# Kernel optimization log

Hardware: AMD Instinct MI355X
Metric: run time of the kernel (lower is better)

Reference implementation:

```python
import jax, jax.numpy as jnp
import numpy as np

H = 2048   # hidden_dim
E = 8      # num_experts
K = 2      # top_k
N = 4096   # tokens


def setup_inputs() -> dict:
    key = jax.random.key(0)
    ks = jax.random.split(key, 8)
    scale = 0.02
    return {
        "x": jax.random.normal(ks[0], (N, H), dtype=jnp.float32),
        # gate: torch Linear(H, E) -> weight [E, H], bias [E]
        "gate_W": jax.random.normal(ks[1], (E, H), dtype=jnp.float32) * scale,
        "gate_b": jnp.zeros((E,), dtype=jnp.float32),
        # per-expert 2-layer MLP; stored as [E, in, out] for direct einsum
        "W1": jax.random.normal(ks[2], (E, H, H), dtype=jnp.float32) * scale,
        "b1": jnp.zeros((E, H), dtype=jnp.float32),
        "W2": jax.random.normal(ks[3], (E, H, H), dtype=jnp.float32) * scale,
        "b2": jnp.zeros((E, H), dtype=jnp.float32),
    }


def reference(x, gate_W, gate_b, W1, b1, W2, b2):
    # gate softmax over experts: [N, E]
    gate_scores = jax.nn.softmax(x @ gate_W.T + gate_b, axis=-1)
    topk_scores, topk_idx = jax.lax.top_k(gate_scores, K)  # [N, K]
    n = x.shape[0]
    # combine weights: score at selected experts, 0 elsewhere -> [N, E]
    combine = jnp.zeros_like(gate_scores).at[
        jnp.arange(n)[:, None], topk_idx
    ].set(topk_scores)
    # dense per-expert MLP: h [N, E, H]
    h = jax.nn.relu(jnp.einsum('nh,ehf->nef', x, W1) + b1)
    out_e = jnp.einsum('nef,efg->neg', h, W2) + b2  # [N, E, H]
    aggregated = jnp.einsum('ne,neh->nh', combine, out_e)  # [N, H]
    return aggregated, gate_scores
```

## Files before the change

### kernel.cpp

```cpp
#include <hip/hip_runtime.h>
#include <hip/hip_bf16.h>

#define N_TOK 4096
#define HD    2048
#define NE    8

#define BM 128
#define BN 256
#define BK 32
#define NKS (HD/BK)
#define MAXROWS (N_TOK*2 + NE*BM)
#define TMAX (MAXROWS/BM)
#define NNT  (HD/BN)
#define NWG  (TMAX*NNT)
#define TSZ  ((BM+BN)*BK*2)

#define NCOPY 64

typedef __attribute__((ext_vector_type(4))) float f32x4;
typedef __attribute__((ext_vector_type(8))) short short8;
typedef __attribute__((ext_vector_type(8))) unsigned short ushort8;

typedef unsigned short u16;
typedef unsigned int   u32;


__device__ __forceinline__ float bf2f(u16 u) {
  union { u32 i; float f; } c; c.i = ((u32)u) << 16; return c.f;
}
__device__ __forceinline__ u16 f2bf(float f) {
  u32 x = __float_as_uint(f);
  u32 r = (x + 0x7fffu + ((x >> 16) & 1u)) >> 16;
  return (u16)r;
}

__device__ __forceinline__ void gload_lds16(const void* gsrc, void* ldst) {
  __builtin_amdgcn_global_load_lds(
      (const __attribute__((address_space(1))) u32*)gsrc,
      (__attribute__((address_space(3))) u32*)ldst, 16, 0, 0);
}

__global__ __launch_bounds__(256) void convert_transpose_kernel(
    const float* __restrict__ W1, const float* __restrict__ W2,
    u16* __restrict__ W1T, u16* __restrict__ W2T) {
  __shared__ float tile[64][257];
  int z = blockIdx.z;
  const float* W = (z < NE) ? W1 : W2;
  u16* WT = (z < NE) ? W1T : W2T;
  int e = z & 7;
  size_t ebase = (size_t)e * HD * HD;
  int n0 = blockIdx.x * 256;
  int k0 = blockIdx.y * 64;
  int t = threadIdx.x;
  int l = t & 63, w = t >> 6;
  #pragma unroll
  for (int i = 0; i < 16; ++i) {
    int r = i*4 + w;
    f32x4 v = *reinterpret_cast<const f32x4*>(W + ebase + (size_t)(k0 + r) * HD + n0 + l*4);
    tile[r][l*4+0] = v[0]; tile[r][l*4+1] = v[1];
    tile[r][l*4+2] = v[2]; tile[r][l*4+3] = v[3];
  }
  __syncthreads();
  #pragma unroll
  for (int i = 0; i < 8; ++i) {
    int np = i*32 + (t >> 3);
    int kc = (t & 7) * 8;
    ushort8 v;
    #pragma unroll
    for (int j = 0; j < 8; ++j) v[j] = f2bf(tile[kc + j][np]);
    *reinterpret_cast<ushort8*>(WT + ebase + (size_t)(n0 + np) * HD + k0 + kc) = v;
  }
}

__global__ __launch_bounds__(256) void gate_kernel(
    const float* __restrict__ x, const float* __restrict__ gW, const float* __restrict__ gb,
    float* __restrict__ gate_out, int* __restrict__ cnt,
    int* __restrict__ picks, float* __restrict__ wts) {
  int wid = (blockIdx.x << 2) + (threadIdx.x >> 6);
  int lane = threadIdx.x & 63;
  int copy = blockIdx.x & (NCOPY-1);
  const float* xr = x + (size_t)wid * HD;
  float s[NE] = {};
  for (int k = 0; k < HD; k += 256) {
    f32x4 xv = *reinterpret_cast<const f32x4*>(xr + k + lane*4);
    #pragma unroll
    for (int e = 0; e < NE; ++e) {
      f32x4 wv = *reinterpret_cast<const f32x4*>(gW + (size_t)e*HD + k + lane*4);
      s[e] += xv[0]*wv[0] + xv[1]*wv[1] + xv[2]*wv[2] + xv[3]*wv[3];
    }
  }
  #pragma unroll
  for (int e = 0; e < NE; ++e) {
    float v = s[e];
    #pragma unroll
    for (int off = 32; off > 0; off >>= 1) v += __shfl_xor(v, off);
    s[e] = v + gb[e];
  }
  float mx = s[0];
  #pragma unroll
  for (int e = 1; e < NE; ++e) mx = fmaxf(mx, s[e]);
  float sum = 0.f;
  #pragma unroll
  for (int e = 0; e < NE; ++e) { s[e] = expf(s[e] - mx); sum += s[e]; }
  float inv = 1.f / sum;
  #pragma unroll
  for (int e = 0; e < NE; ++e) s[e] *= inv;
  int e0 = 0; float v0 = s[0];
  #pragma unroll
  for (int e = 1; e < NE; ++e) if (s[e] > v0) { v0 = s[e]; e0 = e; }
  int e1 = -1; float v1 = -1.f;
  #pragma unroll
  for (int e = 0; e < NE; ++e) if (e != e0 && s[e] > v1) { v1 = s[e]; e1 = e; }
  if (lane == 0) {
    #pragma unroll
    for (int e = 0; e < NE; ++e) gate_out[(size_t)wid*NE + e] = s[e];
    int p0 = atomicAdd(&cnt[copy*8 + e0], 1);
    int p1 = atomicAdd(&cnt[copy*8 + e1], 1);
    picks[wid*2]   = (p0 << 9) | (copy << 3) | e0;
    picks[wid*2+1] = (p1 << 9) | (copy << 3) | e1;
    wts[wid*2]   = v0;
    wts[wid*2+1] = v1;
  }
}

__global__ void scan_kernel(int* meta) {
  int e = threadIdx.x;
  if (e < NE) {
    int run = 0;
    for (int c = 0; c < NCOPY; ++c) {
      meta[512 + c*8 + e] = run;
      run += meta[c*8 + e];
    }
    meta[1024 + e] = run;
  }
}

__global__ void fill_kernel(const int* __restrict__ picks, const int* __restrict__ meta,
                            int* __restrict__ slot, int* __restrict__ rowTok) {
  int i = blockIdx.x * 256 + threadIdx.x;
  if (i >= N_TOK*2) return;
  int p = picks[i];
  int e = p & 7, c = (p >> 3) & (NCOPY-1), pos = p >> 9;
  int base = 0;
  #pragma unroll
  for (int ee = 0; ee < NE; ++ee)
    if (ee < e) base += ((meta[1024+ee] + BM - 1) >> 7) << 7;
  int row = base + meta[512 + c*8 + e] + pos;
  slot[i] = row;
  rowTok[row] = i >> 1;
}

__global__ __launch_bounds__(256) void gather_kernel(
    const float* __restrict__ x, const int* __restrict__ rowTok,
    u16* __restrict__ Xg) {
  int row = blockIdx.x;
  int tok = rowTok[row];
  int c = threadIdx.x * 8;
  ushort8 v;
  if (tok >= 0) {
    const f32x4* src = reinterpret_cast<const f32x4*>(x + (size_t)tok * HD + c);
    f32x4 a = src[0], b = src[1];
    #pragma unroll
    for (int j = 0; j < 4; ++j) { v[j] = f2bf(a[j]); v[4+j] = f2bf(b[j]); }
  } else {
    #pragma unroll
    for (int j = 0; j < 8; ++j) v[j] = 0;
  }
  *reinterpret_cast<ushort8*>(Xg + (size_t)row * HD + c) = v;
}

__device__ __forceinline__ void stage_tile(char* ldsbuf, const u16* Ak, const u16* Bk, int tid) {
  {
    int r = tid >> 2;
    int c = (tid & 3) ^ ((r >> 1) & 3);
    gload_lds16(Ak + (size_t)r*HD + c*8, ldsbuf + tid*16);
  }
  #pragma unroll
  for (int i = 0; i < 2; ++i) {
    int L = i*512 + tid;
    int r = L >> 2;
    int c = (L & 3) ^ ((r >> 1) & 3);
    gload_lds16(Bk + (size_t)r*HD + c*8, ldsbuf + BM*BK*2 + L*16);
  }
}

__device__ __forceinline__ void compute_ktile(
    const char* ldsA, const char* ldsB, f32x4 (&acc)[4][4],
    int wr, int wc, int l15, int lhi) {
  short8 af[4], bfr[4];
  #pragma unroll
  for (int m = 0; m < 4; ++m) {
    int r = wr*64 + m*16 + l15;
    int c = lhi ^ ((r >> 1) & 3);
    af[m] = *reinterpret_cast<const short8*>(ldsA + r*64 + c*16);
  }
  #pragma unroll
  for (int n = 0; n < 4; ++n) {
    int r = wc*64 + n*16 + l15;
    int c = lhi ^ ((r >> 1) & 3);
    bfr[n] = *reinterpret_cast<const short8*>(ldsB + r*64 + c*16);
  }
  #pragma unroll
  for (int m = 0; m < 4; ++m)
    #pragma unroll
    for (int n = 0; n < 4; ++n)
      acc[m][n] = __builtin_amdgcn_mfma_f32_16x16x32_bf16(af[m], bfr[n], acc[m][n], 0, 0, 0);
}

template<bool RELU>
__global__ __launch_bounds__(512, 4) void moe_gemm_kernel(
    const u16* __restrict__ A,
    const u16* __restrict__ WT,
    const float* __restrict__ bias,
    u16* __restrict__ Out,
    const int* __restrict__ tot) {
  int bid = blockIdx.x;
  int wg = (bid & 7) * (NWG/8) + (bid >> 3);
  int t  = wg >> 3;
  int nt = wg & 7;
  int tiles = 0, rows = 0, e = 0, tstart = 0, rbase = 0;
  #pragma unroll
  for (int i = 0; i < NE; ++i) {
    int tl = (tot[i] + BM - 1) >> 7;
    if (t >= tiles && t < tiles + tl) { e = i; tstart = tiles; rbase = rows; }
    tiles += tl; rows += tl << 7;
  }
  if (t >= tiles) return;
  int rowBase = rbase + (t - tstart) * BM;

  const u16* Ap = A + (size_t)rowBase * HD;
  const u16* Bp = WT + ((size_t)e * HD + (size_t)nt * BN) * HD;

  __shared__ char lds[3*TSZ];

  int tid = threadIdx.x;
  int lane = tid & 63;
  int wv = tid >> 6;
  int wr = wv >> 2, wc = wv & 3;
  int l15 = lane & 15, lhi = lane >> 4;

  f32x4 acc[4][4] = {};

  stage_tile(lds,       Ap,      Bp,      tid);
  stage_tile(lds + TSZ, Ap + BK, Bp + BK, tid);

  int rd = 0;
  for (int ks = 0; ks < NKS - 2; ++ks) {
    asm volatile("s_waitcnt vmcnt(3)" ::: "memory");
    __builtin_amdgcn_s_barrier();
    int wi = rd + 2; if (wi >= 3) wi -= 3;
    stage_tile(lds + wi*TSZ, Ap + (ks+2)*BK, Bp + (ks+2)*BK, tid);
    __builtin_amdgcn_sched_barrier(0);
    compute_ktile(lds + rd*TSZ, lds + rd*TSZ + BM*BK*2, acc, wr, wc, l15, lhi);
    if (++rd == 3) rd = 0;
  }
  asm volatile("s_waitcnt vmcnt(3)" ::: "memory");
  __builtin_amdgcn_s_barrier();
  compute_ktile(lds + rd*TSZ, lds + rd*TSZ + BM*BK*2, acc, wr, wc, l15, lhi);
  if (++rd == 3) rd = 0;
  asm volatile("s_waitcnt vmcnt(0)" ::: "memory");
  __builtin_amdgcn_s_barrier();
  compute_ktile(lds + rd*TSZ, lds + rd*TSZ + BM*BK*2, acc, wr, wc, l15, lhi);

  int orow = rowBase + wr*64;
  int ocol = nt*BN + wc*64;
  const float* bp = bias + (size_t)e * HD + ocol;
  #pragma unroll
  for (int n = 0; n < 4; ++n) {
    float bv = bp[n*16 + l15];
    #pragma unroll
    for (int m = 0; m < 4; ++m) {
      #pragma unroll
      for (int j = 0; j < 4; ++j) {
        float v = acc[m][n][j] + bv;
        if (RELU) v = fmaxf(v, 0.f);
        Out[(size_t)(orow + m*16 + lhi*4 + j) * HD + (ocol + n*16 + l15)] = f2bf(v);
      }
    }
  }
}

__global__ __launch_bounds__(256) void combine_kernel(
    const u16* __restrict__ Y, const int* __restrict__ slot,
    const float* __restrict__ wts, float* __restrict__ out) {
  int n = blockIdx.x;
  int r0 = slot[n*2], r1 = slot[n*2+1];
  float w0 = wts[n*2], w1 = wts[n*2+1];
  int c = threadIdx.x * 8;
  ushort8 y0 = *reinterpret_cast<const ushort8*>(Y + (size_t)r0*HD + c);
  ushort8 y1 = *reinterpret_cast<const ushort8*>(Y + (size_t)r1*HD + c);
  f32x4 o0, o1;
  #pragma unroll
  for (int j = 0; j < 4; ++j) {
    o0[j] = w0*bf2f(y0[j])   + w1*bf2f(y1[j]);
    o1[j] = w0*bf2f(y0[4+j]) + w1*bf2f(y1[4+j]);
  }
  f32x4* dst = reinterpret_cast<f32x4*>(out + (size_t)n*HD + c);
  dst[0] = o0; dst[1] = o1;
}

extern "C" void kernel_launch(void* const* d_in, const int* in_sizes, int n_in,
                              void* d_out, int out_size, void* d_ws, size_t ws_size,
                              hipStream_t stream) {
  const float* x     = (const float*)d_in[0];
  const float* gateW = (const float*)d_in[1];
  const float* gateb = (const float*)d_in[2];
  const float* W1    = (const float*)d_in[3];
  const float* b1    = (const float*)d_in[4];
  const float* W2    = (const float*)d_in[5];
  const float* b2    = (const float*)d_in[6];
  float* out      = (float*)d_out;
  float* gate_out = out + (size_t)N_TOK * HD;

  char* ws = (char*)d_ws;
  size_t o = 0;
  u16* W1T = (u16*)(ws + o); o += (size_t)NE*HD*HD*2;
  u16* W2T = (u16*)(ws + o); o += (size_t)NE*HD*HD*2;
  u16* Xg  = (u16*)(ws + o);
  u16* Y   = Xg;
  o += (size_t)MAXROWS*HD*2;
  u16* Hbuf = (u16*)(ws + o); o += (size_t)MAXROWS*HD*2;
  int*   meta   = (int*)(ws + o);   o += 8192;
  int*   picks  = (int*)(ws + o);   o += (size_t)N_TOK*2*4;
  float* wts    = (float*)(ws + o); o += (size_t)N_TOK*2*4;
  int*   slot   = (int*)(ws + o);   o += (size_t)N_TOK*2*4;
  int*   rowTok = (int*)(ws + o);   o += (size_t)MAXROWS*4;

  hipMemsetAsync(meta, 0, NCOPY*8*4, stream);
  hipMemsetAsync(rowTok, 0xFF, (size_t)MAXROWS*4, stream);

  convert_transpose_kernel<<<dim3(HD/256, HD/64, 2*NE), 256, 0, stream>>>(W1, W2, W1T, W2T);
  gate_kernel<<<N_TOK/4, 256, 0, stream>>>(x, gateW, gateb, gate_out, meta, picks, wts);
  scan_kernel<<<1, 64, 0, stream>>>(meta);
  fill_kernel<<<(N_TOK*2)/256, 256, 0, stream>>>(picks, meta, slot, rowTok);
  gather_kernel<<<MAXROWS, 256, 0, stream>>>(x, rowTok, Xg);
  moe_gemm_kernel<true ><<<dim3(NWG), 512, 0, stream>>>(Xg,   W1T, b1, Hbuf, meta + 1024);
  moe_gemm_kernel<false><<<dim3(NWG), 512, 0, stream>>>(Hbuf, W2T, b2, Y,    meta + 1024);
  combine_kernel<<<N_TOK, 256, 0, stream>>>(Y, slot, wts, out);
}
```

Baseline: 323.7 us.

## Fuse weighted combine into second expert GEMM via atomic scatter-add

The separate combine kernel is removed. The second expert GEMM now multiplies each output row by its routing weight and atomically adds the result into the fp32 output at the token's row, which requires zeroing the output buffer with a memset first. This avoids writing and re-reading the bf16 intermediate Y and drops one launch, at the cost of many scattered fp32 atomics and nondeterministic summation order. Separately, the gate kernel now stages the gate weights in LDS before use.

After: 375.8 us. 16.1% more time.

```diff
diff --git a/kernel.cpp b/kernel.cpp
--- a/kernel.cpp
+++ b/kernel.cpp
@@ -76,8 +76,17 @@
     const float* __restrict__ x, const float* __restrict__ gW, const float* __restrict__ gb,
     float* __restrict__ gate_out, int* __restrict__ cnt,
     int* __restrict__ picks, float* __restrict__ wts) {
-  int wid = (blockIdx.x << 2) + (threadIdx.x >> 6);
-  int lane = threadIdx.x & 63;
+  __shared__ float gwl[NE*HD];
+  int tid = threadIdx.x;
+  {
+    const f32x4* g4 = reinterpret_cast<const f32x4*>(gW);
+    f32x4* l4 = reinterpret_cast<f32x4*>(gwl);
+    #pragma unroll
+    for (int i = 0; i < 16; ++i) l4[i*256 + tid] = g4[i*256 + tid];
+  }
+  __syncthreads();
+  int wid = (blockIdx.x << 2) + (tid >> 6);
+  int lane = tid & 63;
   int copy = blockIdx.x & (NCOPY-1);
   const float* xr = x + (size_t)wid * HD;
   float s[NE] = {};
@@ -85,7 +94,7 @@
     f32x4 xv = *reinterpret_cast<const f32x4*>(xr + k + lane*4);
     #pragma unroll
     for (int e = 0; e < NE; ++e) {
-      f32x4 wv = *reinterpret_cast<const f32x4*>(gW + (size_t)e*HD + k + lane*4);
+      f32x4 wv = *reinterpret_cast<const f32x4*>(&gwl[e*HD + k + lane*4]);
       s[e] += xv[0]*wv[0] + xv[1]*wv[1] + xv[2]*wv[2] + xv[3]*wv[3];
     }
   }
@@ -136,7 +145,8 @@
 }
 
 __global__ void fill_kernel(const int* __restrict__ picks, const int* __restrict__ meta,
-                            int* __restrict__ slot, int* __restrict__ rowTok) {
+                            const float* __restrict__ wts,
+                            float* __restrict__ rowW, int* __restrict__ rowTok) {
   int i = blockIdx.x * 256 + threadIdx.x;
   if (i >= N_TOK*2) return;
   int p = picks[i];
@@ -146,7 +156,7 @@
   for (int ee = 0; ee < NE; ++ee)
     if (ee < e) base += ((meta[1024+ee] + BM - 1) >> 7) << 7;
   int row = base + meta[512 + c*8 + e] + pos;
-  slot[i] = row;
+  rowW[row] = wts[i];
   rowTok[row] = i >> 1;
 }
 
@@ -207,13 +217,16 @@
       acc[m][n] = __builtin_amdgcn_mfma_f32_16x16x32_bf16(af[m], bfr[n], acc[m][n], 0, 0, 0);
 }
 
-template<bool RELU>
+template<int MODE>
 __global__ __launch_bounds__(512, 4) void moe_gemm_kernel(
     const u16* __restrict__ A,
     const u16* __restrict__ WT,
     const float* __restrict__ bias,
     u16* __restrict__ Out,
-    const int* __restrict__ tot) {
+    const int* __restrict__ tot,
+    const int* __restrict__ rowTok,
+    const float* __restrict__ rowW,
+    float* __restrict__ fout) {
   int bid = blockIdx.x;
   int wg = (bid & 7) * (NWG/8) + (bid >> 3);
   int t  = wg >> 3;
@@ -265,38 +278,45 @@
   int orow = rowBase + wr*64;
   int ocol = nt*BN + wc*64;
   const float* bp = bias + (size_t)e * HD + ocol;
-  #pragma unroll
-  for (int n = 0; n < 4; ++n) {
-    float bv = bp[n*16 + l15];
-    #pragma unroll
-    for (int m = 0; m < 4; ++m) {
+
+  if (MODE == 0) {
+    #pragma unroll
+    for (int n = 0; n < 4; ++n) {
+      float bv = bp[n*16 + l15];
+      #pragma unroll
+      for (int m = 0; m < 4; ++m) {
+        #pragma unroll
+        for (int j = 0; j < 4; ++j) {
+          float v = fmaxf(acc[m][n][j] + bv, 0.f);
+          Out[(size_t)(orow + m*16 + lhi*4 + j) * HD + (ocol + n*16 + l15)] = f2bf(v);
+        }
+      }
+    }
+  } else {
+    int   tk[4][4];
+    float wk[4][4];
+    #pragma unroll
+    for (int m = 0; m < 4; ++m)
       #pragma unroll
       for (int j = 0; j < 4; ++j) {
-        float v = acc[m][n][j] + bv;
-        if (RELU) v = fmaxf(v, 0.f);
-        Out[(size_t)(orow + m*16 + lhi*4 + j) * HD + (ocol + n*16 + l15)] = f2bf(v);
+        int row = orow + m*16 + lhi*4 + j;
+        tk[m][j] = rowTok[row];
+        wk[m][j] = rowW[row];
+      }
+    #pragma unroll
+    for (int n = 0; n < 4; ++n) {
+      float bv = bp[n*16 + l15];
+      int col = ocol + n*16 + l15;
+      #pragma unroll
+      for (int m = 0; m < 4; ++m) {
+        #pragma unroll
+        for (int j = 0; j < 4; ++j) {
+          if (tk[m][j] >= 0)
+            atomicAdd(&fout[(size_t)tk[m][j] * HD + col], wk[m][j] * (acc[m][n][j] + bv));
+        }
       }
     }
   }
-}
-
-__global__ __launch_bounds__(256) void combine_kernel(
-    const u16* __restrict__ Y, const int* __restrict__ slot,
-    const float* __restrict__ wts, float* __restrict__ out) {
-  int n = blockIdx.x;
-  int r0 = slot[n*2], r1 = slot[n*2+1];
-  float w0 = wts[n*2], w1 = wts[n*2+1];
-  int c = threadIdx.x * 8;
-  ushort8 y0 = *reinterpret_cast<const ushort8*>(Y + (size_t)r0*HD + c);
-  ushort8 y1 = *reinterpret_cast<const ushort8*>(Y + (size_t)r1*HD + c);
-  f32x4 o0, o1;
-  #pragma unroll
-  for (int j = 0; j < 4; ++j) {
-    o0[j] = w0*bf2f(y0[j])   + w1*bf2f(y1[j]);
-    o1[j] = w0*bf2f(y0[4+j]) + w1*bf2f(y1[4+j]);
-  }
-  f32x4* dst = reinterpret_cast<f32x4*>(out + (size_t)n*HD + c);
-  dst[0] = o0; dst[1] = o1;
 }
 
 extern "C" void kernel_launch(void* const* d_in, const int* in_sizes, int n_in,
@@ -316,25 +336,25 @@
   size_t o = 0;
   u16* W1T = (u16*)(ws + o); o += (size_t)NE*HD*HD*2;
   u16* W2T = (u16*)(ws + o); o += (size_t)NE*HD*HD*2;
-  u16* Xg  = (u16*)(ws + o);
-  u16* Y   = Xg;
-  o += (size_t)MAXROWS*HD*2;
+  u16* Xg  = (u16*)(ws + o); o += (size_t)MAXROWS*HD*2;
   u16* Hbuf = (u16*)(ws + o); o += (size_t)MAXROWS*HD*2;
   int*   meta   = (int*)(ws + o);   o += 8192;
   int*   picks  = (int*)(ws + o);   o += (size_t)N_TOK*2*4;
   float* wts    = (float*)(ws + o); o += (size_t)N_TOK*2*4;
-  int*   slot   = (int*)(ws + o);   o += (size_t)N_TOK*2*4;
+  float* rowW   = (float*)(ws + o); o += (size_t)MAXROWS*4;
   int*   rowTok = (int*)(ws + o);   o += (size_t)MAXROWS*4;
 
   hipMemsetAsync(meta, 0, NCOPY*8*4, stream);
   hipMemsetAsync(rowTok, 0xFF, (size_t)MAXROWS*4, stream);
+  hipMemsetAsync(out, 0, (size_t)N_TOK*HD*4, stream);
 
   convert_transpose_kernel<<<dim3(HD/256, HD/64, 2*NE), 256, 0, stream>>>(W1, W2, W1T, W2T);
   gate_kernel<<<N_TOK/4, 256, 0, stream>>>(x, gateW, gateb, gate_out, meta, picks, wts);
   scan_kernel<<<1, 64, 0, stream>>>(meta);
-  fill_kernel<<<(N_TOK*2)/256, 256, 0, stream>>>(picks, meta, slot, rowTok);
+  fill_kernel<<<(N_TOK*2)/256, 256, 0, stream>>>(picks, meta, wts, rowW, rowTok);
   gather_kernel<<<MAXROWS, 256, 0, stream>>>(x, rowTok, Xg);
-  moe_gemm_kernel<true ><<<dim3(NWG), 512, 0, stream>>>(Xg,   W1T, b1, Hbuf, meta + 1024);
-  moe_gemm_kernel<false><<<dim3(NWG), 512, 0, stream>>>(Hbuf, W2T, b2, Y,    meta + 1024);
-  combine_kernel<<<N_TOK, 256, 0, stream>>>(Y, slot, wts, out);
-}
+  moe_gemm_kernel<0><<<dim3(NWG), 512, 0, stream>>>(Xg,   W1T, b1, Hbuf, meta + 1024,
+                                                    rowTok, rowW, out);
+  moe_gemm_kernel<1><<<dim3(NWG), 512, 0, stream>>>(Hbuf, W2T, b2, Hbuf, meta + 1024,
+                                                    rowTok, rowW, out);
+}
```

## Switch expert GEMM to 32x32x16 MFMA and cache gate weights in LDS

Applied to the files above, without the earlier changes.

The expert GEMM inner kernel now uses 32x32x16 bf16 MFMA tiles (2x2 per wave) in place of 16x16x32 tiles (4x4 per wave). Fewer, larger MFMAs cut LDS fragment reads per k-tile and reduce instruction count. The epilogue is remapped to the 32x32 accumulator layout. Separately, the gate kernel stages the full gate weight matrix (64 KB) into shared memory before the dot products, which may reduce occupancy of that small kernel.

After: 331.7 us. 1.02x slower.

```diff
diff --git a/kernel.cpp b/kernel.cpp
--- a/kernel.cpp
+++ b/kernel.cpp
@@ -17,9 +17,10 @@
 
 #define NCOPY 64
 
-typedef __attribute__((ext_vector_type(4))) float f32x4;
-typedef __attribute__((ext_vector_type(8))) short short8;
-typedef __attribute__((ext_vector_type(8))) unsigned short ushort8;
+typedef __attribute__((ext_vector_type(4)))  float f32x4;
+typedef __attribute__((ext_vector_type(16))) float f32x16;
+typedef __attribute__((ext_vector_type(8)))  short short8;
+typedef __attribute__((ext_vector_type(8)))  unsigned short ushort8;
 
 typedef unsigned short u16;
 typedef unsigned int   u32;
@@ -76,8 +77,17 @@
     const float* __restrict__ x, const float* __restrict__ gW, const float* __restrict__ gb,
     float* __restrict__ gate_out, int* __restrict__ cnt,
     int* __restrict__ picks, float* __restrict__ wts) {
-  int wid = (blockIdx.x << 2) + (threadIdx.x >> 6);
-  int lane = threadIdx.x & 63;
+  __shared__ float gwl[NE*HD];
+  int tid = threadIdx.x;
+  {
+    const f32x4* g4 = reinterpret_cast<const f32x4*>(gW);
+    f32x4* l4 = reinterpret_cast<f32x4*>(gwl);
+    #pragma unroll
+    for (int i = 0; i < 16; ++i) l4[i*256 + tid] = g4[i*256 + tid];
+  }
+  __syncthreads();
+  int wid = (blockIdx.x << 2) + (tid >> 6);
+  int lane = tid & 63;
   int copy = blockIdx.x & (NCOPY-1);
   const float* xr = x + (size_t)wid * HD;
   float s[NE] = {};
@@ -85,7 +95,7 @@
     f32x4 xv = *reinterpret_cast<const f32x4*>(xr + k + lane*4);
     #pragma unroll
     for (int e = 0; e < NE; ++e) {
-      f32x4 wv = *reinterpret_cast<const f32x4*>(gW + (size_t)e*HD + k + lane*4);
+      f32x4 wv = *reinterpret_cast<const f32x4*>(&gwl[e*HD + k + lane*4]);
       s[e] += xv[0]*wv[0] + xv[1]*wv[1] + xv[2]*wv[2] + xv[3]*wv[3];
     }
   }
@@ -185,26 +195,29 @@
 }
 
 __device__ __forceinline__ void compute_ktile(
-    const char* ldsA, const char* ldsB, f32x4 (&acc)[4][4],
-    int wr, int wc, int l15, int lhi) {
-  short8 af[4], bfr[4];
-  #pragma unroll
-  for (int m = 0; m < 4; ++m) {
-    int r = wr*64 + m*16 + l15;
-    int c = lhi ^ ((r >> 1) & 3);
-    af[m] = *reinterpret_cast<const short8*>(ldsA + r*64 + c*16);
-  }
-  #pragma unroll
-  for (int n = 0; n < 4; ++n) {
-    int r = wc*64 + n*16 + l15;
-    int c = lhi ^ ((r >> 1) & 3);
-    bfr[n] = *reinterpret_cast<const short8*>(ldsB + r*64 + c*16);
-  }
-  #pragma unroll
-  for (int m = 0; m < 4; ++m)
-    #pragma unroll
-    for (int n = 0; n < 4; ++n)
-      acc[m][n] = __builtin_amdgcn_mfma_f32_16x16x32_bf16(af[m], bfr[n], acc[m][n], 0, 0, 0);
+    const char* ldsA, const char* ldsB, f32x16 (&acc)[2][2],
+    int wr, int wc, int l31, int khalf) {
+  #pragma unroll
+  for (int h = 0; h < 2; ++h) {
+    short8 a2[2], b2[2];
+    #pragma unroll
+    for (int mt = 0; mt < 2; ++mt) {
+      int r = wr*64 + mt*32 + l31;
+      int c = (2*h + khalf) ^ ((r >> 1) & 3);
+      a2[mt] = *reinterpret_cast<const short8*>(ldsA + r*64 + c*16);
+    }
+    #pragma unroll
+    for (int nt2 = 0; nt2 < 2; ++nt2) {
+      int r = wc*64 + nt2*32 + l31;
+      int c = (2*h + khalf) ^ ((r >> 1) & 3);
+      b2[nt2] = *reinterpret_cast<const short8*>(ldsB + r*64 + c*16);
+    }
+    #pragma unroll
+    for (int mt = 0; mt < 2; ++mt)
+      #pragma unroll
+      for (int nt2 = 0; nt2 < 2; ++nt2)
+        acc[mt][nt2] = __builtin_amdgcn_mfma_f32_32x32x16_bf16(a2[mt], b2[nt2], acc[mt][nt2], 0, 0, 0);
+  }
 }
 
 template<bool RELU>
@@ -237,9 +250,9 @@
   int lane = tid & 63;
   int wv = tid >> 6;
   int wr = wv >> 2, wc = wv & 3;
-  int l15 = lane & 15, lhi = lane >> 4;
-
-  f32x4 acc[4][4] = {};
+  int l31 = lane & 31, khalf = lane >> 5;
+
+  f32x16 acc[2][2] = {};
 
   stage_tile(lds,       Ap,      Bp,      tid);
   stage_tile(lds + TSZ, Ap + BK, Bp + BK, tid);
@@ -251,30 +264,31 @@
     int wi = rd + 2; if (wi >= 3) wi -= 3;
     stage_tile(lds + wi*TSZ, Ap + (ks+2)*BK, Bp + (ks+2)*BK, tid);
     __builtin_amdgcn_sched_barrier(0);
-    compute_ktile(lds + rd*TSZ, lds + rd*TSZ + BM*BK*2, acc, wr, wc, l15, lhi);
+    compute_ktile(lds + rd*TSZ, lds + rd*TSZ + BM*BK*2, acc, wr, wc, l31, khalf);
     if (++rd == 3) rd = 0;
   }
   asm volatile("s_waitcnt vmcnt(3)" ::: "memory");
   __builtin_amdgcn_s_barrier();
-  compute_ktile(lds + rd*TSZ, lds + rd*TSZ + BM*BK*2, acc, wr, wc, l15, lhi);
+  compute_ktile(lds + rd*TSZ, lds + rd*TSZ + BM*BK*2, acc, wr, wc, l31, khalf);
   if (++rd == 3) rd = 0;
   asm volatile("s_waitcnt vmcnt(0)" ::: "memory");
   __builtin_amdgcn_s_barrier();
-  compute_ktile(lds + rd*TSZ, lds + rd*TSZ + BM*BK*2, acc, wr, wc, l15, lhi);
+  compute_ktile(lds + rd*TSZ, lds + rd*TSZ + BM*BK*2, acc, wr, wc, l31, khalf);
 
   int orow = rowBase + wr*64;
   int ocol = nt*BN + wc*64;
-  const float* bp = bias + (size_t)e * HD + ocol;
-  #pragma unroll
-  for (int n = 0; n < 4; ++n) {
-    float bv = bp[n*16 + l15];
-    #pragma unroll
-    for (int m = 0; m < 4; ++m) {
+  #pragma unroll
+  for (int mt = 0; mt < 2; ++mt) {
+    #pragma unroll
+    for (int nt2 = 0; nt2 < 2; ++nt2) {
+      int col = ocol + nt2*32 + l31;
+      float bv = bias[(size_t)e * HD + col];
       #pragma unroll
-      for (int j = 0; j < 4; ++j) {
-        float v = acc[m][n][j] + bv;
+      for (int reg = 0; reg < 16; ++reg) {
+        int row = orow + mt*32 + (reg & 3) + 8*(reg >> 2) + 4*khalf;
+        float v = acc[mt][nt2][reg] + bv;
         if (RELU) v = fmaxf(v, 0.f);
-        Out[(size_t)(orow + m*16 + lhi*4 + j) * HD + (ocol + n*16 + l15)] = f2bf(v);
+        Out[(size_t)row * HD + col] = f2bf(v);
       }
     }
   }
```

## Make MoE GEMMs persistent with atomic tile queue and cache gate weights in LDS

Applied to the files above, without the earlier changes.

The two expert GEMM launches now use a fixed grid of 512 persistent workgroups. Each workgroup takes tile indices from an atomic counter until all tiles are consumed, instead of launching one workgroup per possible tile and exiting early on empty ones. The gate kernel copies the full gate weight matrix into shared memory once per block and reads it from there instead of from global memory. The memset is widened to zero the new queue counters. This adds atomic and barrier overhead per tile and heavy LDS use in the gate kernel, which can lower its occupancy.

Result: slower. 410.2 us (+26.7%).

```diff
diff --git a/kernel.cpp b/kernel.cpp
--- a/kernel.cpp
+++ b/kernel.cpp
@@ -13,6 +13,7 @@
 #define TMAX (MAXROWS/BM)
 #define NNT  (HD/BN)
 #define NWG  (TMAX*NNT)
+#define NPB  512
 #define TSZ  ((BM+BN)*BK*2)
 
 #define NCOPY 64
@@ -76,8 +77,17 @@
     const float* __restrict__ x, const float* __restrict__ gW, const float* __restrict__ gb,
     float* __restrict__ gate_out, int* __restrict__ cnt,
     int* __restrict__ picks, float* __restrict__ wts) {
-  int wid = (blockIdx.x << 2) + (threadIdx.x >> 6);
-  int lane = threadIdx.x & 63;
+  __shared__ float gwl[NE*HD];
+  int tid = threadIdx.x;
+  {
+    const f32x4* g4 = reinterpret_cast<const f32x4*>(gW);
+    f32x4* l4 = reinterpret_cast<f32x4*>(gwl);
+    #pragma unroll
+    for (int i = 0; i < 16; ++i) l4[i*256 + tid] = g4[i*256 + tid];
+  }
+  __syncthreads();
+  int wid = (blockIdx.x << 2) + (tid >> 6);
+  int lane = tid & 63;
   int copy = blockIdx.x & (NCOPY-1);
   const float* xr = x + (size_t)wid * HD;
   float s[NE] = {};
@@ -85,7 +95,7 @@
     f32x4 xv = *reinterpret_cast<const f32x4*>(xr + k + lane*4);
     #pragma unroll
     for (int e = 0; e < NE; ++e) {
-      f32x4 wv = *reinterpret_cast<const f32x4*>(gW + (size_t)e*HD + k + lane*4);
+      f32x4 wv = *reinterpret_cast<const f32x4*>(&gwl[e*HD + k + lane*4]);
       s[e] += xv[0]*wv[0] + xv[1]*wv[1] + xv[2]*wv[2] + xv[3]*wv[3];
     }
   }
@@ -213,25 +223,10 @@
     const u16* __restrict__ WT,
     const float* __restrict__ bias,
     u16* __restrict__ Out,
-    const int* __restrict__ tot) {
-  int bid = blockIdx.x;
-  int wg = (bid & 7) * (NWG/8) + (bid >> 3);
-  int t  = wg >> 3;
-  int nt = wg & 7;
-  int tiles = 0, rows = 0, e = 0, tstart = 0, rbase = 0;
-  #pragma unroll
-  for (int i = 0; i < NE; ++i) {
-    int tl = (tot[i] + BM - 1) >> 7;
-    if (t >= tiles && t < tiles + tl) { e = i; tstart = tiles; rbase = rows; }
-    tiles += tl; rows += tl << 7;
-  }
-  if (t >= tiles) return;
-  int rowBase = rbase + (t - tstart) * BM;
-
-  const u16* Ap = A + (size_t)rowBase * HD;
-  const u16* Bp = WT + ((size_t)e * HD + (size_t)nt * BN) * HD;
-
+    const int* __restrict__ tot,
+    int* __restrict__ wq) {
   __shared__ char lds[3*TSZ];
+  __shared__ int tslot;
 
   int tid = threadIdx.x;
   int lane = tid & 63;
@@ -239,42 +234,66 @@
   int wr = wv >> 2, wc = wv & 3;
   int l15 = lane & 15, lhi = lane >> 4;
 
-  f32x4 acc[4][4] = {};
-
-  stage_tile(lds,       Ap,      Bp,      tid);
-  stage_tile(lds + TSZ, Ap + BK, Bp + BK, tid);
-
-  int rd = 0;
-  for (int ks = 0; ks < NKS - 2; ++ks) {
+  while (true) {
+    __syncthreads();
+    if (tid == 0) tslot = atomicAdd(wq, 1);
+    __syncthreads();
+    int wg0 = tslot;
+    if (wg0 >= NWG) break;
+
+    int wg = (wg0 & 7) * (NWG/8) + (wg0 >> 3);
+    int t  = wg >> 3;
+    int nt = wg & 7;
+    int tiles = 0, rows = 0, e = 0, tstart = 0, rbase = 0;
+    #pragma unroll
+    for (int i = 0; i < NE; ++i) {
+      int tl = (tot[i] + BM - 1) >> 7;
+      if (t >= tiles && t < tiles + tl) { e = i; tstart = tiles; rbase = rows; }
+      tiles += tl; rows += tl << 7;
+    }
+    if (t >= tiles) continue;
+    int rowBase = rbase + (t - tstart) * BM;
+
+    const u16* Ap = A + (size_t)rowBase * HD;
+    const u16* Bp = WT + ((size_t)e * HD + (size_t)nt * BN) * HD;
+
+    f32x4 acc[4][4] = {};
+
+    stage_tile(lds,       Ap,      Bp,      tid);
+    stage_tile(lds + TSZ, Ap + BK, Bp + BK, tid);
+
+    int rd = 0;
+    for (int ks = 0; ks < NKS - 2; ++ks) {
+      asm volatile("s_waitcnt vmcnt(3)" ::: "memory");
+      __builtin_amdgcn_s_barrier();
+      int wi = rd + 2; if (wi >= 3) wi -= 3;
+      stage_tile(lds + wi*TSZ, Ap + (ks+2)*BK, Bp + (ks+2)*BK, tid);
+      __builtin_amdgcn_sched_barrier(0);
+      compute_ktile(lds + rd*TSZ, lds + rd*TSZ + BM*BK*2, acc, wr, wc, l15, lhi);
+      if (++rd == 3) rd = 0;
+    }
     asm volatile("s_waitcnt vmcnt(3)" ::: "memory");
     __builtin_amdgcn_s_barrier();
-    int wi = rd + 2; if (wi >= 3) wi -= 3;
-    stage_tile(lds + wi*TSZ, Ap + (ks+2)*BK, Bp + (ks+2)*BK, tid);
-    __builtin_amdgcn_sched_barrier(0);
     compute_ktile(lds + rd*TSZ, lds + rd*TSZ + BM*BK*2, acc, wr, wc, l15, lhi);
     if (++rd == 3) rd = 0;
-  }
-  asm volatile("s_waitcnt vmcnt(3)" ::: "memory");
-  __builtin_amdgcn_s_barrier();
-  compute_ktile(lds + rd*TSZ, lds + rd*TSZ + BM*BK*2, acc, wr, wc, l15, lhi);
-  if (++rd == 3) rd = 0;
-  asm volatile("s_waitcnt vmcnt(0)" ::: "memory");
-  __builtin_amdgcn_s_barrier();
-  compute_ktile(lds + rd*TSZ, lds + rd*TSZ + BM*BK*2, acc, wr, wc, l15, lhi);
-
-  int orow = rowBase + wr*64;
-  int ocol = nt*BN + wc*64;
-  const float* bp = bias + (size_t)e * HD + ocol;
-  #pragma unroll
-  for (int n = 0; n < 4; ++n) {
-    float bv = bp[n*16 + l15];
-    #pragma unroll
-    for (int m = 0; m < 4; ++m) {
+    asm volatile("s_waitcnt vmcnt(0)" ::: "memory");
+    __builtin_amdgcn_s_barrier();
+    compute_ktile(lds + rd*TSZ, lds + rd*TSZ + BM*BK*2, acc, wr, wc, l15, lhi);
+
+    int orow = rowBase + wr*64;
+    int ocol = nt*BN + wc*64;
+    const float* bp = bias + (size_t)e * HD + ocol;
+    #pragma unroll
+    for (int n = 0; n < 4; ++n) {
+      float bv = bp[n*16 + l15];
       #pragma unroll
-      for (int j = 0; j < 4; ++j) {
-        float v = acc[m][n][j] + bv;
-        if (RELU) v = fmaxf(v, 0.f);
-        Out[(size_t)(orow + m*16 + lhi*4 + j) * HD + (ocol + n*16 + l15)] = f2bf(v);
+      for (int m = 0; m < 4; ++m) {
+        #pragma unroll
+        for (int j = 0; j < 4; ++j) {
+          float v = acc[m][n][j] + bv;
+          if (RELU) v = fmaxf(v, 0.f);
+          Out[(size_t)(orow + m*16 + lhi*4 + j) * HD + (ocol + n*16 + l15)] = f2bf(v);
+        }
       }
     }
   }
@@ -326,7 +345,7 @@
   int*   slot   = (int*)(ws + o);   o += (size_t)N_TOK*2*4;
   int*   rowTok = (int*)(ws + o);   o += (size_t)MAXROWS*4;
 
-  hipMemsetAsync(meta, 0, NCOPY*8*4, stream);
+  hipMemsetAsync(meta, 0, 4352, stream);
   hipMemsetAsync(rowTok, 0xFF, (size_t)MAXROWS*4, stream);
 
   convert_transpose_kernel<<<dim3(HD/256, HD/64, 2*NE), 256, 0, stream>>>(W1, W2, W1T, W2T);
@@ -334,7 +353,7 @@
   scan_kernel<<<1, 64, 0, stream>>>(meta);
   fill_kernel<<<(N_TOK*2)/256, 256, 0, stream>>>(picks, meta, slot, rowTok);
   gather_kernel<<<MAXROWS, 256, 0, stream>>>(x, rowTok, Xg);
-  moe_gemm_kernel<true ><<<dim3(NWG), 512, 0, stream>>>(Xg,   W1T, b1, Hbuf, meta + 1024);
-  moe_gemm_kernel<false><<<dim3(NWG), 512, 0, stream>>>(Hbuf, W2T, b2, Y,    meta + 1024);
+  moe_gemm_kernel<true ><<<dim3(NPB), 512, 0, stream>>>(Xg,   W1T, b1, Hbuf, meta + 1024, meta + 1032);
+  moe_gemm_kernel<false><<<dim3(NPB), 512, 0, stream>>>(Hbuf, W2T, b2, Y,    meta + 1024, meta + 1033);
   combine_kernel<<<N_TOK, 256, 0, stream>>>(Y, slot, wts, out);
 }
```
